# Kernel tuning notes

Hardware: AMD Instinct MI355X
Metric: run time of the kernel (lower is better)

The kernel has to match this reference:

```python
import jax, jax.numpy as jnp
import numpy as np

EPS = 1e-8
L_TEMEL, L_DENGE, L_CPU, L_SURU, L_NASH = 1.0, 0.1, 0.05, 0.03, 0.02


def setup_inputs() -> dict:
    key = jax.random.key(0)
    ks = jax.random.split(key, 8)
    N_tok, V = 8192, 32000
    N_birim, D, K = 100000, 64, 16
    return {
        "tahminler": jax.random.normal(ks[0], (N_tok, V), dtype=jnp.float32),
        "hedefler": jax.random.randint(ks[1], (N_tok,), 0, V),
        "is_yuku_dagilimi": jax.random.uniform(ks[2], (N_birim,), dtype=jnp.float32),
        "onbellek_durumu": jax.random.uniform(ks[3], (N_birim,), dtype=jnp.float32),
        "secilen_indeksler": jax.random.randint(ks[4], (N_tok,), 0, N_birim),
        "birim_stratejileri": jax.random.normal(ks[5], (N_birim, D), dtype=jnp.float32),
        "komsu_indeksleri": jax.random.randint(ks[6], (N_birim, K), 0, N_birim),
        "oyuncu_kazanimlari": jax.random.uniform(ks[7], (N_birim,), dtype=jnp.float32),
        "mevcut_stratejiler": jax.random.normal(jax.random.fold_in(key, 99), (N_birim, D), dtype=jnp.float32),
    }


def _var_mean_ratio(x):
    # torch.var is unbiased (ddof=1)
    return jnp.var(x, ddof=1) / (jnp.mean(x) + EPS)


def _suru_uyum(strat, komsu_idx):
    # strat: [N, D], komsu_idx: [N, K]
    komsu = strat[komsu_idx]                 # [N, K, D] ragged-gather (uniform degree)
    ort_komsu = jnp.mean(komsu, axis=1)      # [N, D]
    bn = jnp.linalg.norm(strat, axis=-1)     # [N]
    kn = jnp.linalg.norm(ort_komsu, axis=-1) # [N]
    dots = jnp.einsum("nd,nd->n", strat, ort_komsu)
    valid = (bn > EPS) & (kn > EPS)
    cos = jnp.where(valid, dots / jnp.where(valid, bn * kn, 1.0), 0.0)
    cnt = jnp.sum(valid)
    uyum = jnp.where(cnt > 0, jnp.sum(cos) / jnp.maximum(cnt, 1), 0.0)
    return (uyum + 1.0) / 2.0


def reference(tahminler, hedefler, is_yuku_dagilimi, onbellek_durumu,
              secilen_indeksler, birim_stratejileri, komsu_indeksleri,
              oyuncu_kazanimlari, mevcut_stratejiler):
    # 1) CrossEntropyLoss (mean over tokens)
    logp = jax.nn.log_softmax(tahminler, axis=-1)
    temel = -jnp.take_along_axis(logp, hedefler[:, None], axis=1).mean()
    # 2) workload balance: var/mean
    dengeleme = _var_mean_ratio(is_yuku_dagilimi)
    # 3) cache hit-rate on selected indices
    cpu = jnp.mean(onbellek_durumu[secilen_indeksler])
    # 4) swarm cohesion via neighbor cosine similarity
    suru = _suru_uyum(birim_stratejileri, komsu_indeksleri)
    # 5) Nash regularization: var/mean of payoffs (mevcut_stratejiler unused, as in torch)
    nash = _var_mean_ratio(oyuncu_kazanimlari)
    toplam = (L_TEMEL * temel + L_DENGE * dengeleme - L_CPU * cpu
              - L_SURU * suru + L_NASH * nash)
    return jnp.stack([toplam, temel, dengeleme, cpu, suru, nash])
```

## Files before the change

kernel.cpp:

```cpp
#include <hip/hip_runtime.h>
#include <hip/hip_bf16.h>

#define WS_CE 0
#define WS_YSUM 1
#define WS_YSQ 2
#define WS_GATHER 3
#define WS_COS 4
#define WS_CNT 5
#define WS_OSUM 6
#define WS_OSQ 7

#define SURU_BLOCKS 256
#define STAT_BLOCKS 64
#define GATHER_BLOCKS 32
#define PRE_BLOCKS (SURU_BLOCKS + 2 * STAT_BLOCKS + GATHER_BLOCKS)
#define CE_BLOCKS 2048

typedef float f32x4 __attribute__((ext_vector_type(4)));

__device__ __forceinline__ float wave_sum(float v) {
#pragma unroll
    for (int off = 32; off > 0; off >>= 1) v += __shfl_xor(v, off, 64);
    return v;
}

__global__ void init_ws_kernel(float* ws) {
    if (threadIdx.x < 8) ws[threadIdx.x] = 0.f;
}

__global__ __launch_bounds__(256, 8) void fused_kernel(
    const float* __restrict__ logits, const int* __restrict__ targets, int V, int n_tok,
    const float* __restrict__ yuku, const float* __restrict__ oyun, int n_birim,
    const float* __restrict__ onbellek, const int* __restrict__ secilen,
    const float* __restrict__ strat, const int* __restrict__ komsu, int K,
    float* ws) {
    __shared__ float sh_a[4], sh_b[4];
    const int b = blockIdx.x;
    const int wid = threadIdx.x >> 6;
    const int lane = threadIdx.x & 63;

    if (b >= PRE_BLOCKS) {
        const int nvec = V >> 2;
        const int nmain = nvec & ~1023;
        const int base = wid * 256 + lane;
        float ce_local = 0.f;
        for (int row = b - PRE_BLOCKS; row < n_tok; row += CE_BLOCKS) {
            const float* rowp = logits + (size_t)row * V;
            const f32x4* rp = (const f32x4*)rowp;
            float s0 = 0.f, s1 = 0.f, s2 = 0.f, s3 = 0.f;
            for (int t = 0; t < nmain; t += 1024) {
                const f32x4* p = rp + t + base;
                f32x4 v0 = p[0];
                f32x4 v1 = p[64];
                f32x4 v2 = p[128];
                f32x4 v3 = p[192];
                s0 += __expf(v0.x); s1 += __expf(v0.y); s2 += __expf(v0.z); s3 += __expf(v0.w);
                s0 += __expf(v1.x); s1 += __expf(v1.y); s2 += __expf(v1.z); s3 += __expf(v1.w);
                s0 += __expf(v2.x); s1 += __expf(v2.y); s2 += __expf(v2.z); s3 += __expf(v2.w);
                s0 += __expf(v3.x); s1 += __expf(v3.y); s2 += __expf(v3.z); s3 += __expf(v3.w);
            }
            for (int v = nmain + (int)threadIdx.x; v < nvec; v += 256) {
                f32x4 x = rp[v];
                s0 += __expf(x.x); s1 += __expf(x.y); s2 += __expf(x.z); s3 += __expf(x.w);
            }
            float s = (s0 + s1) + (s2 + s3);
            s = wave_sum(s);
            if (lane == 0) sh_a[wid] = s;
            __syncthreads();
            if (threadIdx.x == 0) {
                float S = sh_a[0] + sh_a[1] + sh_a[2] + sh_a[3];
                float xt = rowp[targets[row]];
                ce_local += logf(S) - xt;
            }
            __syncthreads();
        }
        if (threadIdx.x == 0 && ce_local != 0.f)
            atomicAdd(ws + WS_CE, ce_local);
        return;
    }

    if (b < SURU_BLOCKS) {
        const int nwave = SURU_BLOCKS * 4;
        float cos_sum = 0.f, cnt = 0.f;
        if (K == 16) {
            for (int u = b * 4 + wid; u < n_birim; u += nwave) {
                float own = strat[(size_t)u * 64 + lane];
                const int* kp = komsu + (size_t)u * 16;
                float acc = 0.f;
#pragma unroll
                for (int h = 0; h < 2; ++h) {
                    int idx[8];
#pragma unroll
                    for (int k = 0; k < 8; ++k) idx[k] = kp[h * 8 + k];
                    float g[8];
#pragma unroll
                    for (int k = 0; k < 8; ++k) g[k] = strat[(size_t)idx[k] * 64 + lane];
#pragma unroll
                    for (int k = 0; k < 8; ++k) acc += g[k];
                }
                float ort = acc * (1.f / 16.f);
                float dot = wave_sum(own * ort);
                float b2 = wave_sum(own * own);
                float k2 = wave_sum(ort * ort);
                float bn = sqrtf(b2), knrm = sqrtf(k2);
                if (bn > 1e-8f && knrm > 1e-8f) {
                    cos_sum += dot / (bn * knrm);
                    cnt += 1.f;
                }
            }
        } else {
            for (int u = b * 4 + wid; u < n_birim; u += nwave) {
                float own = strat[(size_t)u * 64 + lane];
                const int* kp = komsu + (size_t)u * K;
                float acc = 0.f;
                for (int k = 0; k < K; ++k)
                    acc += strat[(size_t)kp[k] * 64 + lane];
                float ort = acc / (float)K;
                float dot = wave_sum(own * ort);
                float b2 = wave_sum(own * own);
                float k2 = wave_sum(ort * ort);
                float bn = sqrtf(b2), knrm = sqrtf(k2);
                if (bn > 1e-8f && knrm > 1e-8f) {
                    cos_sum += dot / (bn * knrm);
                    cnt += 1.f;
                }
            }
        }
        if (lane == 0) { sh_a[wid] = cos_sum; sh_b[wid] = cnt; }
        __syncthreads();
        if (threadIdx.x == 0) {
            atomicAdd(ws + WS_COS, sh_a[0] + sh_a[1] + sh_a[2] + sh_a[3]);
            atomicAdd(ws + WS_CNT, sh_b[0] + sh_b[1] + sh_b[2] + sh_b[3]);
        }
        return;
    }

    if (b < SURU_BLOCKS + 2 * STAT_BLOCKS) {
        const int sb = b - SURU_BLOCKS;
        const bool is_oyun = sb >= STAT_BLOCKS;
        const int sbb = is_oyun ? sb - STAT_BLOCKS : sb;
        const float* x = is_oyun ? oyun : yuku;
        const int sum_idx = is_oyun ? WS_OSUM : WS_YSUM;
        const int sq_idx = is_oyun ? WS_OSQ : WS_YSQ;
        float s = 0.f, sq = 0.f;
        for (int i = sbb * 256 + threadIdx.x; i < n_birim; i += STAT_BLOCKS * 256) {
            float v = x[i];
            s += v;
            sq += v * v;
        }
        s = wave_sum(s);
        sq = wave_sum(sq);
        if (lane == 0) { sh_a[wid] = s; sh_b[wid] = sq; }
        __syncthreads();
        if (threadIdx.x == 0) {
            atomicAdd(ws + sum_idx, sh_a[0] + sh_a[1] + sh_a[2] + sh_a[3]);
            atomicAdd(ws + sq_idx, sh_b[0] + sh_b[1] + sh_b[2] + sh_b[3]);
        }
        return;
    }

    {
        const int gb = b - SURU_BLOCKS - 2 * STAT_BLOCKS;
        float s = 0.f;
        for (int i = gb * 256 + threadIdx.x; i < n_tok; i += GATHER_BLOCKS * 256)
            s += onbellek[secilen[i]];
        s = wave_sum(s);
        if (lane == 0) sh_a[wid] = s;
        __syncthreads();
        if (threadIdx.x == 0)
            atomicAdd(ws + WS_GATHER, sh_a[0] + sh_a[1] + sh_a[2] + sh_a[3]);
    }
}

__global__ void finalize_kernel(const float* __restrict__ ws, float* __restrict__ out,
                                int n_tok, int n_birim) {
    if (threadIdx.x != 0 || blockIdx.x != 0) return;
    const float n = (float)n_birim;
    float temel = ws[WS_CE] / (float)n_tok;

    float ysum = ws[WS_YSUM];
    float ymean = ysum / n;
    float yvar = (ws[WS_YSQ] - ysum * ysum / n) / (n - 1.f);
    float denge = yvar / (ymean + 1e-8f);

    float cpu = ws[WS_GATHER] / (float)n_tok;

    float cnt = ws[WS_CNT];
    float uyum = cnt > 0.f ? ws[WS_COS] / fmaxf(cnt, 1.f) : 0.f;
    float suru = (uyum + 1.f) * 0.5f;

    float osum = ws[WS_OSUM];
    float omean = osum / n;
    float ovar = (ws[WS_OSQ] - osum * osum / n) / (n - 1.f);
    float nash = ovar / (omean + 1e-8f);

    float toplam = 1.0f * temel + 0.1f * denge - 0.05f * cpu - 0.03f * suru + 0.02f * nash;
    out[0] = toplam;
    out[1] = temel;
    out[2] = denge;
    out[3] = cpu;
    out[4] = suru;
    out[5] = nash;
}

extern "C" void kernel_launch(void* const* d_in, const int* in_sizes, int n_in,
                              void* d_out, int out_size, void* d_ws, size_t ws_size,
                              hipStream_t stream) {
    const float* tahminler = (const float*)d_in[0];
    const int* hedefler = (const int*)d_in[1];
    const float* yuku = (const float*)d_in[2];
    const float* onbellek = (const float*)d_in[3];
    const int* secilen = (const int*)d_in[4];
    const float* strat = (const float*)d_in[5];
    const int* komsu = (const int*)d_in[6];
    const float* oyun = (const float*)d_in[7];

    const int n_tok = in_sizes[1];
    const int V = in_sizes[0] / n_tok;
    const int n_birim = in_sizes[2];
    const int K = in_sizes[6] / n_birim;

    float* ws = (float*)d_ws;
    float* out = (float*)d_out;

    init_ws_kernel<<<1, 64, 0, stream>>>(ws);
    fused_kernel<<<PRE_BLOCKS + CE_BLOCKS, 256, 0, stream>>>(
        tahminler, hedefler, V, n_tok,
        yuku, oyun, n_birim,
        onbellek, secilen,
        strat, komsu, K, ws);
    finalize_kernel<<<1, 64, 0, stream>>>(ws, out, n_tok, n_birim);
}
```

Measured before the change: 269.2 us.

## Process one CE row per wave and place auxiliary blocks after CE

The cross-entropy part now gives each wavefront its own row: 2048 blocks of four waves, with no __syncthreads and an atomicAdd per row. The old scheme had a grid-stride loop where a whole block reduced each row through shared memory. Logit loads use nontemporal hints, and the small auxiliary blocks (cohesion, stats, gather) now come after the CE blocks instead of before. The aim is to remove block-level barriers and to stream the big logits array without polluting the cache. The cost is 8192 global atomics on one address and longer serial per-wave loops.

```diff
diff --git a/kernel.cpp b/kernel.cpp
--- a/kernel.cpp
+++ b/kernel.cpp
@@ -13,8 +13,7 @@
 #define SURU_BLOCKS 256
 #define STAT_BLOCKS 64
 #define GATHER_BLOCKS 32
-#define PRE_BLOCKS (SURU_BLOCKS + 2 * STAT_BLOCKS + GATHER_BLOCKS)
-#define CE_BLOCKS 2048
+#define POST_BLOCKS (SURU_BLOCKS + 2 * STAT_BLOCKS + GATHER_BLOCKS)
 
 typedef float f32x4 __attribute__((ext_vector_type(4)));
 
@@ -38,52 +37,43 @@
     const int b = blockIdx.x;
     const int wid = threadIdx.x >> 6;
     const int lane = threadIdx.x & 63;
-
-    if (b >= PRE_BLOCKS) {
+    const int ce_blocks = (n_tok + 3) >> 2;
+
+    if (b < ce_blocks) {
+        const int row = b * 4 + wid;
+        if (row >= n_tok) return;
+        const float* rowp = logits + (size_t)row * V;
+        const f32x4* rp = (const f32x4*)rowp;
         const int nvec = V >> 2;
-        const int nmain = nvec & ~1023;
-        const int base = wid * 256 + lane;
-        float ce_local = 0.f;
-        for (int row = b - PRE_BLOCKS; row < n_tok; row += CE_BLOCKS) {
-            const float* rowp = logits + (size_t)row * V;
-            const f32x4* rp = (const f32x4*)rowp;
-            float s0 = 0.f, s1 = 0.f, s2 = 0.f, s3 = 0.f;
-            for (int t = 0; t < nmain; t += 1024) {
-                const f32x4* p = rp + t + base;
-                f32x4 v0 = p[0];
-                f32x4 v1 = p[64];
-                f32x4 v2 = p[128];
-                f32x4 v3 = p[192];
-                s0 += __expf(v0.x); s1 += __expf(v0.y); s2 += __expf(v0.z); s3 += __expf(v0.w);
-                s0 += __expf(v1.x); s1 += __expf(v1.y); s2 += __expf(v1.z); s3 += __expf(v1.w);
-                s0 += __expf(v2.x); s1 += __expf(v2.y); s2 += __expf(v2.z); s3 += __expf(v2.w);
-                s0 += __expf(v3.x); s1 += __expf(v3.y); s2 += __expf(v3.z); s3 += __expf(v3.w);
-            }
-            for (int v = nmain + (int)threadIdx.x; v < nvec; v += 256) {
-                f32x4 x = rp[v];
-                s0 += __expf(x.x); s1 += __expf(x.y); s2 += __expf(x.z); s3 += __expf(x.w);
-            }
-            float s = (s0 + s1) + (s2 + s3);
-            s = wave_sum(s);
-            if (lane == 0) sh_a[wid] = s;
-            __syncthreads();
-            if (threadIdx.x == 0) {
-                float S = sh_a[0] + sh_a[1] + sh_a[2] + sh_a[3];
-                float xt = rowp[targets[row]];
-                ce_local += logf(S) - xt;
-            }
-            __syncthreads();
-        }
-        if (threadIdx.x == 0 && ce_local != 0.f)
-            atomicAdd(ws + WS_CE, ce_local);
+        float s0 = 0.f, s1 = 0.f, s2 = 0.f, s3 = 0.f;
+        int i = lane;
+        for (; i + 192 < nvec; i += 256) {
+            f32x4 v0 = __builtin_nontemporal_load(rp + i);
+            f32x4 v1 = __builtin_nontemporal_load(rp + i + 64);
+            f32x4 v2 = __builtin_nontemporal_load(rp + i + 128);
+            f32x4 v3 = __builtin_nontemporal_load(rp + i + 192);
+            s0 += __expf(v0.x); s1 += __expf(v0.y); s2 += __expf(v0.z); s3 += __expf(v0.w);
+            s0 += __expf(v1.x); s1 += __expf(v1.y); s2 += __expf(v1.z); s3 += __expf(v1.w);
+            s0 += __expf(v2.x); s1 += __expf(v2.y); s2 += __expf(v2.z); s3 += __expf(v2.w);
+            s0 += __expf(v3.x); s1 += __expf(v3.y); s2 += __expf(v3.z); s3 += __expf(v3.w);
+        }
+        for (; i < nvec; i += 64) {
+            f32x4 v = __builtin_nontemporal_load(rp + i);
+            s0 += __expf(v.x); s1 += __expf(v.y); s2 += __expf(v.z); s3 += __expf(v.w);
+        }
+        float s = wave_sum((s0 + s1) + (s2 + s3));
+        if (lane == 0)
+            atomicAdd(ws + WS_CE, logf(s) - rowp[targets[row]]);
         return;
     }
 
-    if (b < SURU_BLOCKS) {
+    const int pb = b - ce_blocks;
+
+    if (pb < SURU_BLOCKS) {
         const int nwave = SURU_BLOCKS * 4;
         float cos_sum = 0.f, cnt = 0.f;
         if (K == 16) {
-            for (int u = b * 4 + wid; u < n_birim; u += nwave) {
+            for (int u = pb * 4 + wid; u < n_birim; u += nwave) {
                 float own = strat[(size_t)u * 64 + lane];
                 const int* kp = komsu + (size_t)u * 16;
                 float acc = 0.f;
@@ -109,7 +99,7 @@
                 }
             }
         } else {
-            for (int u = b * 4 + wid; u < n_birim; u += nwave) {
+            for (int u = pb * 4 + wid; u < n_birim; u += nwave) {
                 float own = strat[(size_t)u * 64 + lane];
                 const int* kp = komsu + (size_t)u * K;
                 float acc = 0.f;
@@ -135,8 +125,8 @@
         return;
     }
 
-    if (b < SURU_BLOCKS + 2 * STAT_BLOCKS) {
-        const int sb = b - SURU_BLOCKS;
+    if (pb < SURU_BLOCKS + 2 * STAT_BLOCKS) {
+        const int sb = pb - SURU_BLOCKS;
         const bool is_oyun = sb >= STAT_BLOCKS;
         const int sbb = is_oyun ? sb - STAT_BLOCKS : sb;
         const float* x = is_oyun ? oyun : yuku;
@@ -160,7 +150,7 @@
     }
 
     {
-        const int gb = b - SURU_BLOCKS - 2 * STAT_BLOCKS;
+        const int gb = pb - SURU_BLOCKS - 2 * STAT_BLOCKS;
         float s = 0.f;
         for (int i = gb * 256 + threadIdx.x; i < n_tok; i += GATHER_BLOCKS * 256)
             s += onbellek[secilen[i]];
@@ -223,8 +213,10 @@
     float* ws = (float*)d_ws;
     float* out = (float*)d_out;
 
+    const int ce_blocks = (n_tok + 3) / 4;
+
     init_ws_kernel<<<1, 64, 0, stream>>>(ws);
-    fused_kernel<<<PRE_BLOCKS + CE_BLOCKS, 256, 0, stream>>>(
+    fused_kernel<<<ce_blocks + POST_BLOCKS, 256, 0, stream>>>(
         tahminler, hedefler, V, n_tok,
         yuku, oyun, n_birim,
         onbellek, secilen,
```

New measurement: 320.7 us. 19.1% more time.
